# Kernel optimization log

Hardware: AMD Instinct MI355X
Metric: run time of the kernel (lower is better)

## Reference

```python
import jax, jax.numpy as jnp
import numpy as np

OUT, IN = 4096, 4096          # weight_shape
T, K, GROUP = 256, 2, 256     # trellis window, bits/weight, weight_scales_group_size
GRID = np.array([-3.0, -1.0, 1.0, 3.0], dtype=np.float32) / np.sqrt(5.0)  # 2-bit symmetric, unit-power


def fwht(x):
    """Normalized fast Walsh-Hadamard transform along the last axis (H = H^T, orthonormal)."""
    n = x.shape[-1]
    orig = x.shape
    y = x.reshape(-1, n)
    rows = y.shape[0]
    h = 1
    while h < n:
        y = y.reshape(rows, n // (2 * h), 2, h)
        a, b = y[:, :, 0, :], y[:, :, 1, :]
        y = jnp.stack([a + b, a - b], axis=2)
        h *= 2
    return y.reshape(orig) * (1.0 / np.sqrt(n)).astype(np.float32)


def fake_quant_u8_per_channel(x):
    """InputQuantizer: 8-bit PER_CHANNEL asymmetric fake-quant over the last (in-channel) dim."""
    red = tuple(range(x.ndim - 1))
    xmin = jnp.min(x, axis=red)
    xmax = jnp.max(x, axis=red)
    scale = jnp.maximum((xmax - xmin) / 255.0, 1e-8)
    zero = jnp.round(-xmin / scale)
    q = jnp.clip(jnp.round(x / scale) + zero, 0.0, 255.0)
    dq = (q - zero) * scale
    # straight-through estimator (matches torch fake-quant training behavior)
    return x + jax.lax.stop_gradient(dq - x)


def decode_trellis(trellis):
    """LowBitSym decode: unpack K=2-bit codes from packed 16-bit trellis words and map
    to the symmetric unit-power 2-bit grid. trellis: (NV, T//16*K) int -> (OUT, IN) float."""
    shifts = jnp.arange(14, -1, -2, dtype=jnp.int32)         # MSB-first 2-bit fields
    codes = (trellis[:, :, None] >> shifts) & 3               # (NV, 32, 8)
    grid = jnp.asarray(GRID)
    return grid[codes].reshape(OUT, IN)


def setup_inputs() -> dict:
    key = jax.random.key(0)
    k1, k2, k3, k4, k5 = jax.random.split(key, 5)
    x = jax.random.normal(k1, (4, 2048, IN), dtype=jnp.float32)
    SU = jax.random.normal(k2, (IN,), dtype=jnp.float32)
    SV = jax.random.normal(k3, (OUT,), dtype=jnp.float32)
    weight_scales = jax.random.uniform(k4, (OUT * IN // GROUP, 1), dtype=jnp.float32)
    trellis = jax.random.randint(k5, (OUT * IN // T, T // 16 * K), 0, 65536, dtype=jnp.int32)
    return {"x": x, "SU": SU, "SV": SV, "weight_scales": weight_scales, "trellis": trellis}


def reference(x, SU, SV, weight_scales, trellis):
    # activation path: incoherence rotate + 8-bit fake quant
    xh = fwht(x * SU)                       # matmul_hadUt_cuda(x * SU)
    xq = fake_quant_u8_per_channel(xh)
    # weight path: trellis decode + Hadamard + SV + grouped scales
    w = decode_trellis(trellis)             # (OUT, IN)
    w = (fwht(w.T) * SV).T                  # (matmul_hadU_cuda(w.T) * SV).T
    w = (w.reshape(-1, GROUP) * weight_scales).reshape(OUT, IN)
    # F.linear(input=xq, weight=w)
    return jnp.einsum('bsi,oi->bso', xq, w)
```

## Files before the change

### kernel.cpp

```cpp
#include <hip/hip_runtime.h>
#include <hip/hip_bf16.h>
#include <stdint.h>

#define IN_DIM 4096
#define OUT_DIM 4096
#define M_ROWS 8192

typedef __attribute__((ext_vector_type(8))) short s16x8;
typedef __attribute__((ext_vector_type(4))) float f32x4;

__device__ __forceinline__ unsigned short f2bf(float f) {
  uint32_t u = __float_as_uint(f);
  uint32_t r = (u + 0x7fffu + ((u >> 16) & 1u)) >> 16;
  return (unsigned short)r;
}
__device__ __forceinline__ float b2f(unsigned short u) {
  return __uint_as_float((uint32_t)u << 16);
}

__device__ __forceinline__ void async16(void* lds, const void* g) {
  __builtin_amdgcn_global_load_lds(
      (const __attribute__((address_space(1))) unsigned int*)g,
      (__attribute__((address_space(3))) unsigned int*)lds, 16, 0, 0);
}

#define FENCE asm volatile("" ::: "memory")

__device__ __forceinline__ void h16(float (&v)[16]) {
#pragma unroll
  for (int h = 1; h < 16; h <<= 1) {
#pragma unroll
    for (int g = 0; g < 8; ++g) {
      int r = g & (h - 1);
      int i0 = ((g & ~(h - 1)) << 1) | r;
      float a = v[i0], b = v[i0 + h];
      v[i0] = a + b;
      v[i0 + h] = a - b;
    }
  }
}

__global__ void fwht_x_kernel(const float* __restrict__ x, const float* __restrict__ SU,
                              unsigned short* __restrict__ xh) {
  __shared__ float s[4352];
  const int row = blockIdx.x;
  const int t = threadIdx.x;
  float v[16];
  const float* xr = x + (size_t)row * IN_DIM;
#pragma unroll
  for (int a = 0; a < 16; ++a) {
    int i = a * 256 + t;
    v[a] = xr[i] * SU[i];
  }
  h16(v);
#pragma unroll
  for (int a = 0; a < 16; ++a) {
    int i = a * 256 + t;
    s[i + (i >> 4)] = v[a];
  }
  __syncthreads();
  const int A = t >> 4, C = t & 15;
#pragma unroll
  for (int b = 0; b < 16; ++b) {
    int i = A * 256 + b * 16 + C;
    v[b] = s[i + (i >> 4)];
  }
  h16(v);
  __syncthreads();
#pragma unroll
  for (int b = 0; b < 16; ++b) {
    int i = A * 256 + b * 16 + C;
    s[i + (i >> 4)] = v[b];
  }
  __syncthreads();
#pragma unroll
  for (int c = 0; c < 16; ++c) {
    int i = t * 16 + c;
    v[c] = s[i + (i >> 4)];
  }
  h16(v);
  unsigned short ob[16];
#pragma unroll
  for (int c = 0; c < 16; ++c) ob[c] = f2bf(v[c] * 0.015625f);
  s16x8* dst = (s16x8*)(xh + (size_t)row * IN_DIM + t * 16);
  dst[0] = *(s16x8*)&ob[0];
  dst[1] = *(s16x8*)&ob[8];
}

__global__ void minmax_part_kernel(const unsigned short* __restrict__ xh,
                                   float* __restrict__ pmin, float* __restrict__ pmax) {
  const int rc = blockIdx.x >> 3;
  const int cb = blockIdx.x & 7;
  const int ch0 = cb * 512 + threadIdx.x * 2;
  float mn0 = 3.4e38f, mx0 = -3.4e38f, mn1 = 3.4e38f, mx1 = -3.4e38f;
  const unsigned int* base =
      (const unsigned int*)(xh + (size_t)rc * 256 * IN_DIM + ch0);
  for (int r = 0; r < 256; ++r) {
    unsigned int u = base[(size_t)r * (IN_DIM / 2)];
    float v0 = __uint_as_float(u << 16);
    float v1 = __uint_as_float(u & 0xffff0000u);
    mn0 = fminf(mn0, v0); mx0 = fmaxf(mx0, v0);
    mn1 = fminf(mn1, v1); mx1 = fmaxf(mx1, v1);
  }
  pmin[rc * IN_DIM + ch0] = mn0;
  pmin[rc * IN_DIM + ch0 + 1] = mn1;
  pmax[rc * IN_DIM + ch0] = mx0;
  pmax[rc * IN_DIM + ch0 + 1] = mx1;
}

__global__ void minmax_fin_kernel(const float* __restrict__ pmin, const float* __restrict__ pmax,
                                  float* __restrict__ scale, float* __restrict__ zero) {
  int ch = blockIdx.x * 256 + threadIdx.x;
  float mn = 3.4e38f, mx = -3.4e38f;
  for (int rc = 0; rc < 32; ++rc) {
    mn = fminf(mn, pmin[rc * IN_DIM + ch]);
    mx = fmaxf(mx, pmax[rc * IN_DIM + ch]);
  }
  float sc = fmaxf((mx - mn) / 255.0f, 1e-8f);
  float zp = rintf(-mn / sc);
  scale[ch] = sc;
  zero[ch] = zp;
}

__global__ void quant_kernel(const unsigned short* __restrict__ xh,
                             const float* __restrict__ scale, const float* __restrict__ zero,
                             unsigned short* __restrict__ xq) {
  const int total8 = M_ROWS * IN_DIM / 8;
  for (int i8 = blockIdx.x * blockDim.x + threadIdx.x; i8 < total8;
       i8 += gridDim.x * blockDim.x) {
    int c8 = i8 & (IN_DIM / 8 - 1);
    s16x8 v = ((const s16x8*)xh)[i8];
    unsigned short o[8];
#pragma unroll
    for (int j = 0; j < 8; ++j) {
      float sc = scale[c8 * 8 + j];
      float zp = zero[c8 * 8 + j];
      float f = b2f((unsigned short)v[j]);
      float q = fminf(fmaxf(rintf(f / sc) + zp, 0.f), 255.f);
      o[j] = f2bf((q - zp) * sc);
    }
    ((s16x8*)xq)[i8] = *(s16x8*)&o[0];
  }
}

#define W_RADIX4(TARR)                                                     \
  for (int h = 1; h < 64; h <<= 2) {                                       \
    __syncthreads();                                                       \
    _Pragma("unroll") for (int j = 0; j < 4; ++j) {                        \
      int g = j * 256 + tid;                                               \
      int c = g & 63, u = g >> 6;                                          \
      int r = u & (h - 1);                                                 \
      int i0 = ((u & ~(h - 1)) << 2) | r;                                  \
      float a = TARR[i0][c], b2 = TARR[i0 + h][c];                         \
      float c2 = TARR[i0 + 2 * h][c], d = TARR[i0 + 3 * h][c];             \
      float y0 = a + b2, y1 = a - b2, y2 = c2 + d, y3 = c2 - d;            \
      TARR[i0][c] = y0 + y2;                                               \
      TARR[i0 + h][c] = y1 + y3;                                           \
      TARR[i0 + 2 * h][c] = y0 - y2;                                       \
      TARR[i0 + 3 * h][c] = y1 - y3;                                       \
    }                                                                      \
  }                                                                        \
  __syncthreads();

__global__ void fwht_w_inner_fused(const int* __restrict__ trellis,
                                   unsigned short* __restrict__ w) {
  __shared__ float t[64][65];
  const int ohi = blockIdx.x >> 6;
  const int it  = blockIdx.x & 63;
  const int tid = threadIdx.x;
  const float g = 0.44721359549995793f;
#pragma unroll
  for (int j = 0; j < 2; ++j) {
    int wi = j * 256 + tid;
    int r = wi >> 3, wc = wi & 7;
    int word = trellis[(size_t)(ohi * 64 + r) * 512 + it * 8 + wc];
#pragma unroll
    for (int jj = 0; jj < 8; ++jj) {
      int code = (word >> (14 - 2 * jj)) & 3;
      t[r][wc * 8 + jj] = (float)(2 * code - 3) * g;
    }
  }
  W_RADIX4(t)
#pragma unroll
  for (int j = 0; j < 16; ++j) {
    int e = j * 256 + tid;
    int r = e >> 6, c = e & 63;
    w[((size_t)(ohi * 64 + r)) * IN_DIM + it * 64 + c] = f2bf(t[r][c]);
  }
}

__global__ void fwht_w_outer(const unsigned short* __restrict__ w,
                             const float* __restrict__ SV,
                             const float* __restrict__ wscale, unsigned short* __restrict__ wq) {
  __shared__ float t[64][65];
  const int olo = blockIdx.x >> 6;
  const int it  = blockIdx.x & 63;
  const int tid = threadIdx.x;
#pragma unroll
  for (int j = 0; j < 16; ++j) {
    int e = j * 256 + tid;
    int r = e >> 6, c = e & 63;
    t[r][c] = b2f(w[((size_t)(r * 64 + olo)) * IN_DIM + it * 64 + c]);
  }
  W_RADIX4(t)
#pragma unroll
  for (int j = 0; j < 16; ++j) {
    int e = j * 256 + tid;
    int r = e >> 6, c = e & 63;
    int o = r * 64 + olo;
    int i = it * 64 + c;
    float val = t[r][c] * 0.015625f * SV[o] * wscale[(o << 4) + (i >> 8)];
    wq[(size_t)o * IN_DIM + i] = f2bf(val);
  }
}

__global__ __launch_bounds__(512, 2) void gemm256_kernel(
    const unsigned short* __restrict__ A, const unsigned short* __restrict__ B,
    float* __restrict__ C) {
  __shared__ __align__(16) unsigned short lds[65536];
  const int tid  = threadIdx.x;
  const int lane = tid & 63;
  const int wave = tid >> 6;
  const int wm = wave >> 2, wn = wave & 3;
  const int fr = lane & 15, kqi = lane >> 4;
  const int swz = fr & 7;

  const int b  = blockIdx.x;
  const int wg = (b & 7) * 64 + (b >> 3);
  const int bm = wg >> 4, bn = wg & 15;
  const int gm0 = bm * 256, gn0 = bn * 256;

  f32x4 acc[2][2][4][2] = {};
  s16x8 af[4][2];
  s16x8 bf[2][2][2];

  const int F0 = tid, F1 = 512 + tid;
  const int rh0 = F0 >> 3, s0 = (F0 & 7) ^ (rh0 & 7);
  const int rh1 = F1 >> 3, s1 = (F1 & 7) ^ (rh1 & 7);
  auto stage = [&](const unsigned short* gbase, int grow0, int kcol, int ldsoff) {
    async16((void*)&lds[ldsoff + F0 * 8],
            (const void*)(gbase + (size_t)(grow0 + rh0) * IN_DIM + kcol + s0 * 8));
    async16((void*)&lds[ldsoff + F1 * 8],
            (const void*)(gbase + (size_t)(grow0 + rh1) * IN_DIM + kcol + s1 * 8));
  };

#define READ_AF(QM, TBUF)                                                                \
  {                                                                                      \
    const int abase = (TBUF) * 16384 + (QM) * 8192;                                      \
    _Pragma("unroll") for (int kk = 0; kk < 2; ++kk)                                     \
      _Pragma("unroll") for (int mi = 0; mi < 4; ++mi) {                                 \
        int rh = wm * 64 + mi * 16 + fr;                                                 \
        af[mi][kk] = *(const s16x8*)&lds[abase + rh * 64 + (((kk * 4 + kqi) ^ swz) * 8)];\
      }                                                                                  \
  }
#define READ_BF(QN, TBUF)                                                                \
  {                                                                                      \
    const int bbase = 32768 + (TBUF) * 16384 + (QN) * 8192;                              \
    _Pragma("unroll") for (int kk = 0; kk < 2; ++kk)                                     \
      _Pragma("unroll") for (int ni = 0; ni < 2; ++ni) {                                 \
        int rh = wn * 32 + ni * 16 + fr;                                                 \
        bf[QN][ni][kk] =                                                                 \
            *(const s16x8*)&lds[bbase + rh * 64 + (((kk * 4 + kqi) ^ swz) * 8)];         \
      }                                                                                  \
  }
#define ENDPHASE(QM, QN, SGBASE, SGROW0, SKCOL, SLDSOFF, VM)                             \
  {                                                                                      \
    stage(SGBASE, SGROW0, SKCOL, SLDSOFF);                                               \
    FENCE;                                                                               \
    asm volatile("s_waitcnt vmcnt(" #VM ")" ::: "memory");                               \
    __builtin_amdgcn_s_barrier();                                                        \
    FENCE;                                                                               \
    __builtin_amdgcn_s_setprio(1);                                                       \
    _Pragma("unroll") for (int kk = 0; kk < 2; ++kk)                                     \
      _Pragma("unroll") for (int mi = 0; mi < 4; ++mi)                                   \
        _Pragma("unroll") for (int ni = 0; ni < 2; ++ni)                                 \
          acc[QM][QN][mi][ni] = __builtin_amdgcn_mfma_f32_16x16x32_bf16(                 \
              af[mi][kk], bf[QN][ni][kk], acc[QM][QN][mi][ni], 0, 0, 0);                 \
    __builtin_amdgcn_s_setprio(0);                                                       \
    FENCE;                                                                               \
    __builtin_amdgcn_s_barrier();                                                        \
    FENCE;                                                                               \
  }

  stage(A, gm0,       0, 0);
  stage(B, gn0,       0, 32768);
  stage(A, gm0 + 128, 0, 8192);
  stage(B, gn0 + 128, 0, 40960);
  stage(A, gm0,      64, 16384);
  stage(B, gn0,      64, 49152);
  FENCE;
  asm volatile("s_waitcnt vmcnt(8)" ::: "memory");
  __builtin_amdgcn_s_barrier();
  FENCE;

  for (int it = 0; it < 32; ++it) {
    const int k1 = ((2 * it + 1) * 64) & 4095;
    const int k2 = ((2 * it + 2) * 64) & 4095;
    const int k3 = ((2 * it + 3) * 64) & 4095;
    READ_AF(0, 0) READ_BF(0, 0)
    ENDPHASE(0, 0, A, gm0 + 128, k1, 24576, 6)
    READ_BF(1, 0)
    ENDPHASE(0, 1, B, gn0 + 128, k1, 57344, 63)
    READ_AF(1, 0)
    ENDPHASE(1, 1, A, gm0,       k2, 0,     63)
    ENDPHASE(1, 0, B, gn0,       k2, 32768, 8)
    READ_AF(0, 1) READ_BF(0, 1)
    ENDPHASE(0, 0, A, gm0 + 128, k2, 8192,  6)
    READ_BF(1, 1)
    ENDPHASE(0, 1, B, gn0 + 128, k2, 40960, 63)
    READ_AF(1, 1)
    ENDPHASE(1, 1, A, gm0,       k3, 16384, 63)
    ENDPHASE(1, 0, B, gn0,       k3, 49152, 8)
  }
#undef ENDPHASE
#undef READ_AF
#undef READ_BF
  asm volatile("s_waitcnt vmcnt(0)" ::: "memory");

  const int orow = kqi * 4;
#pragma unroll
  for (int qm = 0; qm < 2; ++qm)
#pragma unroll
    for (int qn = 0; qn < 2; ++qn)
#pragma unroll
      for (int mi = 0; mi < 4; ++mi)
#pragma unroll
        for (int ni = 0; ni < 2; ++ni) {
          const int row0 = gm0 + qm * 128 + wm * 64 + mi * 16 + orow;
          const int col  = gn0 + qn * 128 + wn * 32 + ni * 16 + fr;
          f32x4 v = acc[qm][qn][mi][ni];
#pragma unroll
          for (int r = 0; r < 4; ++r)
            C[(size_t)(row0 + r) * OUT_DIM + col] = v[r];
        }
}

extern "C" void kernel_launch(void* const* d_in, const int* in_sizes, int n_in,
                              void* d_out, int out_size, void* d_ws, size_t ws_size,
                              hipStream_t stream) {
  const float* x      = (const float*)d_in[0];
  const float* SU     = (const float*)d_in[1];
  const float* SV     = (const float*)d_in[2];
  const float* wscale = (const float*)d_in[3];
  const int* trellis  = (const int*)d_in[4];
  float* out = (float*)d_out;

  char* ws = (char*)d_ws;
  unsigned short* xq = (unsigned short*)ws;
  unsigned short* wq = (unsigned short*)(ws + (size_t)67108864);
  float* pmin  = (float*)(ws + (size_t)67108864);
  float* pmax  = (float*)(ws + (size_t)67108864 + 524288);
  float* scale = (float*)(ws + (size_t)67108864 + 1048576);
  float* zero  = (float*)(ws + (size_t)67108864 + 1064960);

  unsigned short* xh   = (unsigned short*)out;
  unsigned short* wdec = (unsigned short*)out + (size_t)33554432;

  hipLaunchKernelGGL(fwht_x_kernel, dim3(M_ROWS), dim3(256), 0, stream, x, SU, xh);
  hipLaunchKernelGGL(minmax_part_kernel, dim3(256), dim3(256), 0, stream, xh, pmin, pmax);
  hipLaunchKernelGGL(minmax_fin_kernel, dim3(16), dim3(256), 0, stream, pmin, pmax, scale, zero);
  hipLaunchKernelGGL(quant_kernel, dim3(2048), dim3(256), 0, stream, xh, scale, zero, xq);
  hipLaunchKernelGGL(fwht_w_inner_fused, dim3(4096), dim3(256), 0, stream, trellis, wdec);
  hipLaunchKernelGGL(fwht_w_outer, dim3(4096), dim3(256), 0, stream, wdec, SV, wscale, wq);
  hipLaunchKernelGGL(gemm256_kernel, dim3((M_ROWS / 256) * (OUT_DIM / 256)), dim3(512), 0,
                     stream, xq, wq, out);
}
```

Baseline: 344.1 us.

## Double-buffer fragment registers to overlap LDS reads with MFMA phases

Splits the A/B register fragments into two sets and issues LDS reads for the next phase inside the current phase's MFMA block, between the barriers. This hides LDS read latency behind matrix instructions instead of serializing reads before each phase. It raises VGPR pressure, which could cause spills under the 512x2 launch bounds. Reads placed before barriers also need correct ordering against the async LDS staging writes.

```diff
diff --git a/kernel.cpp b/kernel.cpp
--- a/kernel.cpp
+++ b/kernel.cpp
@@ -231,8 +231,8 @@
   const int gm0 = bm * 256, gn0 = bn * 256;
 
   f32x4 acc[2][2][4][2] = {};
-  s16x8 af[4][2];
-  s16x8 bf[2][2][2];
+  s16x8 af0[4][2], af1[4][2];
+  s16x8 bf0[2][2], bf1[2][2];
 
   const int F0 = tid, F1 = 512 + tid;
   const int rh0 = F0 >> 3, s0 = (F0 & 7) ^ (rh0 & 7);
@@ -244,43 +244,40 @@
             (const void*)(gbase + (size_t)(grow0 + rh1) * IN_DIM + kcol + s1 * 8));
   };
 
-#define READ_AF(QM, TBUF)                                                                \
-  {                                                                                      \
-    const int abase = (TBUF) * 16384 + (QM) * 8192;                                      \
-    _Pragma("unroll") for (int kk = 0; kk < 2; ++kk)                                     \
-      _Pragma("unroll") for (int mi = 0; mi < 4; ++mi) {                                 \
-        int rh = wm * 64 + mi * 16 + fr;                                                 \
-        af[mi][kk] = *(const s16x8*)&lds[abase + rh * 64 + (((kk * 4 + kqi) ^ swz) * 8)];\
-      }                                                                                  \
-  }
-#define READ_BF(QN, TBUF)                                                                \
-  {                                                                                      \
-    const int bbase = 32768 + (TBUF) * 16384 + (QN) * 8192;                              \
-    _Pragma("unroll") for (int kk = 0; kk < 2; ++kk)                                     \
-      _Pragma("unroll") for (int ni = 0; ni < 2; ++ni) {                                 \
-        int rh = wn * 32 + ni * 16 + fr;                                                 \
-        bf[QN][ni][kk] =                                                                 \
-            *(const s16x8*)&lds[bbase + rh * 64 + (((kk * 4 + kqi) ^ swz) * 8)];         \
-      }                                                                                  \
-  }
-#define ENDPHASE(QM, QN, SGBASE, SGROW0, SKCOL, SLDSOFF, VM)                             \
-  {                                                                                      \
-    stage(SGBASE, SGROW0, SKCOL, SLDSOFF);                                               \
-    FENCE;                                                                               \
-    asm volatile("s_waitcnt vmcnt(" #VM ")" ::: "memory");                               \
-    __builtin_amdgcn_s_barrier();                                                        \
-    FENCE;                                                                               \
-    __builtin_amdgcn_s_setprio(1);                                                       \
-    _Pragma("unroll") for (int kk = 0; kk < 2; ++kk)                                     \
-      _Pragma("unroll") for (int mi = 0; mi < 4; ++mi)                                   \
-        _Pragma("unroll") for (int ni = 0; ni < 2; ++ni)                                 \
-          acc[QM][QN][mi][ni] = __builtin_amdgcn_mfma_f32_16x16x32_bf16(                 \
-              af[mi][kk], bf[QN][ni][kk], acc[QM][QN][mi][ni], 0, 0, 0);                 \
-    __builtin_amdgcn_s_setprio(0);                                                       \
-    FENCE;                                                                               \
-    __builtin_amdgcn_s_barrier();                                                        \
-    FENCE;                                                                               \
-  }
+#define READ_AF2(DST, QM, TBUF, MIH)                                                      \
+  {                                                                                       \
+    const int abase = (TBUF) * 16384 + (QM) * 8192;                                       \
+    _Pragma("unroll") for (int kk = 0; kk < 2; ++kk)                                      \
+      _Pragma("unroll") for (int mi = 2 * (MIH); mi < 2 * (MIH) + 2; ++mi) {              \
+        int rh = wm * 64 + mi * 16 + fr;                                                  \
+        DST[mi][kk] = *(const s16x8*)&lds[abase + rh * 64 + (((kk * 4 + kqi) ^ swz) * 8)];\
+      }                                                                                   \
+  }
+#define READ_BF2(DST, QN, TBUF, NI)                                                       \
+  {                                                                                       \
+    const int bbase = 32768 + (TBUF) * 16384 + (QN) * 8192;                               \
+    const int rh = wn * 32 + (NI) * 16 + fr;                                              \
+    _Pragma("unroll") for (int kk = 0; kk < 2; ++kk)                                      \
+      DST[NI][kk] = *(const s16x8*)&lds[bbase + rh * 64 + (((kk * 4 + kqi) ^ swz) * 8)];  \
+  }
+#define MFMA16(QM, QN, AF, BF)                                                            \
+    _Pragma("unroll") for (int kk = 0; kk < 2; ++kk)                                      \
+      _Pragma("unroll") for (int mi = 0; mi < 4; ++mi)                                    \
+        _Pragma("unroll") for (int ni = 0; ni < 2; ++ni)                                  \
+          acc[QM][QN][mi][ni] = __builtin_amdgcn_mfma_f32_16x16x32_bf16(                  \
+              AF[mi][kk], BF[ni][kk], acc[QM][QN][mi][ni], 0, 0, 0);
+#define PHASE_BEGIN(SGBASE, SGROW0, SKCOL, SLDSOFF, VM)                                   \
+    stage(SGBASE, SGROW0, SKCOL, SLDSOFF);                                                \
+    FENCE;                                                                                \
+    asm volatile("s_waitcnt vmcnt(" #VM ")" ::: "memory");                                \
+    __builtin_amdgcn_s_barrier();                                                         \
+    FENCE;                                                                                \
+    __builtin_amdgcn_s_setprio(1);
+#define PHASE_END                                                                         \
+    __builtin_amdgcn_s_setprio(0);                                                        \
+    FENCE;                                                                                \
+    __builtin_amdgcn_s_barrier();                                                         \
+    FENCE;
 
   stage(A, gm0,       0, 0);
   stage(B, gn0,       0, 32768);
@@ -292,29 +289,53 @@
   asm volatile("s_waitcnt vmcnt(8)" ::: "memory");
   __builtin_amdgcn_s_barrier();
   FENCE;
+  READ_AF2(af0, 0, 0, 0)
+  READ_BF2(bf0, 0, 0, 0)
 
   for (int it = 0; it < 32; ++it) {
     const int k1 = ((2 * it + 1) * 64) & 4095;
     const int k2 = ((2 * it + 2) * 64) & 4095;
     const int k3 = ((2 * it + 3) * 64) & 4095;
-    READ_AF(0, 0) READ_BF(0, 0)
-    ENDPHASE(0, 0, A, gm0 + 128, k1, 24576, 6)
-    READ_BF(1, 0)
-    ENDPHASE(0, 1, B, gn0 + 128, k1, 57344, 63)
-    READ_AF(1, 0)
-    ENDPHASE(1, 1, A, gm0,       k2, 0,     63)
-    ENDPHASE(1, 0, B, gn0,       k2, 32768, 8)
-    READ_AF(0, 1) READ_BF(0, 1)
-    ENDPHASE(0, 0, A, gm0 + 128, k2, 8192,  6)
-    READ_BF(1, 1)
-    ENDPHASE(0, 1, B, gn0 + 128, k2, 40960, 63)
-    READ_AF(1, 1)
-    ENDPHASE(1, 1, A, gm0,       k3, 16384, 63)
-    ENDPHASE(1, 0, B, gn0,       k3, 49152, 8)
-  }
-#undef ENDPHASE
-#undef READ_AF
-#undef READ_BF
+    READ_AF2(af0, 0, 0, 1) READ_BF2(bf0, 0, 0, 1)
+    PHASE_BEGIN(A, gm0 + 128, k1, 24576, 6)
+    MFMA16(0, 0, af0, bf0)
+    READ_BF2(bf1, 1, 0, 0) READ_BF2(bf1, 1, 0, 1)
+    PHASE_END
+    PHASE_BEGIN(B, gn0 + 128, k1, 57344, 63)
+    MFMA16(0, 1, af0, bf1)
+    READ_AF2(af1, 1, 0, 0)
+    PHASE_END
+    READ_AF2(af1, 1, 0, 1)
+    PHASE_BEGIN(A, gm0,       k2, 0,     63)
+    MFMA16(1, 1, af1, bf1)
+    PHASE_END
+    PHASE_BEGIN(B, gn0,       k2, 32768, 8)
+    MFMA16(1, 0, af1, bf0)
+    READ_AF2(af0, 0, 1, 0) READ_BF2(bf0, 0, 1, 0)
+    PHASE_END
+    READ_AF2(af0, 0, 1, 1) READ_BF2(bf0, 0, 1, 1)
+    PHASE_BEGIN(A, gm0 + 128, k2, 8192,  6)
+    MFMA16(0, 0, af0, bf0)
+    READ_BF2(bf1, 1, 1, 0) READ_BF2(bf1, 1, 1, 1)
+    PHASE_END
+    PHASE_BEGIN(B, gn0 + 128, k2, 40960, 63)
+    MFMA16(0, 1, af0, bf1)
+    READ_AF2(af1, 1, 1, 0)
+    PHASE_END
+    READ_AF2(af1, 1, 1, 1)
+    PHASE_BEGIN(A, gm0,       k3, 16384, 63)
+    MFMA16(1, 1, af1, bf1)
+    PHASE_END
+    PHASE_BEGIN(B, gn0,       k3, 49152, 8)
+    MFMA16(1, 0, af1, bf0)
+    READ_AF2(af0, 0, 0, 0) READ_BF2(bf0, 0, 0, 0)
+    PHASE_END
+  }
+#undef PHASE_BEGIN
+#undef PHASE_END
+#undef MFMA16
+#undef READ_AF2
+#undef READ_BF2
   asm volatile("s_waitcnt vmcnt(0)" ::: "memory");
 
   const int orow = kqi * 4;
```

Result: faster. 336.2 us (-2.3%).
